# Optimization experiments

Hardware: AMD Instinct MI355X
Metric: run time of the kernel (lower is better)

Reference implementation:

```python
import jax, jax.numpy as jnp
import numpy as np

N_NODES = 20000
N_EDGES = 640000
D = 128          # vision_dim == topo_dim
OUT = 256        # out_dim
B = 64           # image batch == num graphs
HW = 64
NEG_SLOPE = 0.2


def _sn(w2d, u):
    """PyTorch spectral_norm forward: one power iteration (u,v detached), W/sigma."""
    v = jax.lax.stop_gradient(w2d.T @ u)
    v = v / (jnp.linalg.norm(v) + 1e-12)
    u2 = jax.lax.stop_gradient(w2d @ v)
    u2 = u2 / (jnp.linalg.norm(u2) + 1e-12)
    sigma = u2 @ (w2d @ v)
    return w2d / sigma


def _leaky(x):
    return jnp.where(x >= 0, x, NEG_SLOPE * x)


def setup_inputs() -> dict:
    key = jax.random.key(0)
    ks = jax.random.split(key, 16)
    vis = jax.random.normal(ks[0], (B, D, HW, HW), dtype=jnp.float32)
    topo = jax.random.normal(ks[1], (N_NODES, D), dtype=jnp.float32)
    edge_index = jax.random.randint(ks[2], (2, N_EDGES), 0, N_NODES, dtype=jnp.int64)
    batch = jnp.sort(jax.random.randint(ks[3], (N_NODES,), 0, B, dtype=jnp.int64))
    s = 0.05
    conv_w = jax.random.normal(ks[4], (D, D, 3, 3), dtype=jnp.float32) * s
    conv_b = jnp.zeros((D,), dtype=jnp.float32)
    conv_u = jax.random.normal(ks[5], (D,), dtype=jnp.float32)
    fcv_w = jax.random.normal(ks[6], (OUT, D * 4), dtype=jnp.float32) * s
    fcv_b = jnp.zeros((OUT,), dtype=jnp.float32)
    fcv_u = jax.random.normal(ks[7], (OUT,), dtype=jnp.float32)
    gcn_w = jax.random.normal(ks[8], (D, D), dtype=jnp.float32) * s
    gcn_b = jnp.zeros((D,), dtype=jnp.float32)
    fct_w = jax.random.normal(ks[9], (OUT, D), dtype=jnp.float32) * s
    fct_b = jnp.zeros((OUT,), dtype=jnp.float32)
    fct_u = jax.random.normal(ks[10], (OUT,), dtype=jnp.float32)
    return dict(vis=vis, topo=topo, edge_index=edge_index, batch=batch,
                conv_w=conv_w, conv_b=conv_b, conv_u=conv_u,
                fcv_w=fcv_w, fcv_b=fcv_b, fcv_u=fcv_u,
                gcn_w=gcn_w, gcn_b=gcn_b,
                fct_w=fct_w, fct_b=fct_b, fct_u=fct_u)


def reference(vis, topo, edge_index, batch,
              conv_w, conv_b, conv_u,
              fcv_w, fcv_b, fcv_u,
              gcn_w, gcn_b,
              fct_w, fct_b, fct_u):
    # ---- vision head: spectral-norm conv3x3 -> leaky_relu -> adaptive max pool 2x2 -> SN linear
    cw = _sn(conv_w.reshape(D, -1), conv_u).reshape(conv_w.shape)
    x = jax.lax.conv_general_dilated(vis, cw, window_strides=(1, 1), padding='VALID',
                                     dimension_numbers=('NCHW', 'OIHW', 'NCHW'))
    x = _leaky(x + conv_b[None, :, None, None])              # [B, D, 62, 62]
    Bc, C, H, W = x.shape
    x = x.reshape(Bc, C, 2, H // 2, 2, W // 2).max(axis=(3, 5))  # adaptive max pool -> [B,D,2,2]
    x = x.reshape(Bc, -1)                                    # [B, 4D]
    vis_score = x @ _sn(fcv_w, fcv_u).T + fcv_b              # [B, OUT]

    # ---- topo head: GCNConv (sym-norm, self-loops) -> leaky_relu -> global max pool -> SN linear
    n = topo.shape[0]
    loop = jnp.arange(n, dtype=edge_index.dtype)
    src = jnp.concatenate([edge_index[0], loop])
    dst = jnp.concatenate([edge_index[1], loop])
    deg = jax.ops.segment_sum(jnp.ones_like(dst, dtype=topo.dtype), dst, num_segments=n)
    dis = jnp.where(deg > 0, jax.lax.rsqrt(jnp.maximum(deg, 1.0)), 0.0)
    norm = dis[src] * dis[dst]                               # [E+N]
    xw = topo @ gcn_w                                        # [N, D]
    h = jax.ops.segment_sum(norm[:, None] * xw[src], dst, num_segments=n) + gcn_b
    h = _leaky(h)
    pooled = jax.ops.segment_max(h, batch, num_segments=B)   # [B, D]
    topo_score = pooled @ _sn(fct_w, fct_u).T + fct_b        # [B, OUT]

    return (vis_score, topo_score)
```

## Files before the change

kernel.cpp:

```cpp
#include <hip/hip_runtime.h>
#include <hip/hip_bf16.h>
#include <float.h>
#include <stdint.h>

#define NB   64
#define CD   128
#define OUTD 256
#define NNODE 20000
#define NEDGE 640000

typedef __bf16 bf16x8 __attribute__((ext_vector_type(8)));
typedef __bf16 bf16x4 __attribute__((ext_vector_type(4)));
typedef float  f32x4  __attribute__((ext_vector_type(4)));

__device__ inline void gl_lds16(const void* g, void* l) {
  __builtin_amdgcn_global_load_lds(
      (const __attribute__((address_space(1))) void*)g,
      (__attribute__((address_space(3))) void*)l, 16, 0, 0);
}

__device__ inline void atomicMaxF(float* addr, float val) {
  if (val >= 0.f) atomicMax((int*)addr, __float_as_int(val));
  else            atomicMin((unsigned int*)addr, __float_as_uint(val));
}

__global__ void k_init(float* __restrict__ pooled_v, float* __restrict__ pooled_t,
                       int* __restrict__ cnt, int* __restrict__ fill,
                       float* __restrict__ sn_scratch, int* __restrict__ ntotal) {
  const int i = blockIdx.x * 256 + threadIdx.x;
  if (i < NB * CD * 4) pooled_v[i] = -FLT_MAX;
  if (i < NB * CD)     pooled_t[i] = -FLT_MAX;
  if (i < NNODE)       { cnt[i] = 0; fill[i] = 0; }
  if (i < 1796)        sn_scratch[i] = 0.0f;
  if (i == 0)          *ntotal = 0;
}

__global__ __launch_bounds__(256) void k_sn_v(const float* __restrict__ conv_w, const float* __restrict__ conv_u,
                                              const float* __restrict__ fcv_w,  const float* __restrict__ fcv_u,
                                              const float* __restrict__ fct_w,  const float* __restrict__ fct_u,
                                              float* __restrict__ sn) {
  const int bb = blockIdx.x;
  const float* W; const float* u; float* v; int C; int r0;
  if (bb < 4)       { W = conv_w; u = conv_u; v = sn;        C = 1152; r0 = bb * 32; }
  else if (bb < 12) { W = fcv_w;  u = fcv_u;  v = sn + 1152; C = 512;  r0 = (bb - 4) * 32; }
  else              { W = fct_w;  u = fct_u;  v = sn + 1664; C = 128;  r0 = (bb - 12) * 32; }
  const int tid = threadIdx.x;
  float acc[5] = {0.f, 0.f, 0.f, 0.f, 0.f};
  for (int i = r0; i < r0 + 32; ++i) {
    const float ui = u[i];
    const float* row = W + (size_t)i * C;
    #pragma unroll
    for (int t = 0; t < 5; ++t) {
      const int j = tid + t * 256;
      if (j < C) acc[t] += ui * row[j];
    }
  }
  #pragma unroll
  for (int t = 0; t < 5; ++t) {
    const int j = tid + t * 256;
    if (j < C) atomicAdd(&v[j], acc[t]);
  }
}

__global__ __launch_bounds__(256) void k_sn_w(const float* __restrict__ conv_w,
                                              const float* __restrict__ fcv_w,
                                              const float* __restrict__ fct_w,
                                              float* __restrict__ sn) {
  const int gw = blockIdx.x * 4 + (threadIdx.x >> 6);
  const int lane = threadIdx.x & 63;
  const float* W; const float* v; int C, m, row;
  if (gw < 128)      { W = conv_w; v = sn;        C = 1152; m = 0; row = gw; }
  else if (gw < 384) { W = fcv_w;  v = sn + 1152; C = 512;  m = 1; row = gw - 128; }
  else               { W = fct_w;  v = sn + 1664; C = 128;  m = 2; row = gw - 384; }
  const float* wr = W + (size_t)row * C;
  float y = 0.f;
  for (int c = lane; c < C; c += 64) y += wr[c] * v[c];
  #pragma unroll
  for (int s = 32; s > 0; s >>= 1) y += __shfl_xor(y, s, 64);
  if (lane == 0) atomicAdd(&sn[1792 + m], y * y);
}

__global__ __launch_bounds__(256) void k_sn_fin(const float* __restrict__ sn, float* __restrict__ inv_sigma) {
  __shared__ float red[256];
  const int tid = threadIdx.x;
  const int off[4] = {0, 1152, 1664, 1792};
  for (int m = 0; m < 3; ++m) {
    const int C = off[m + 1] - off[m];
    float ss = 0.f;
    for (int j = tid; j < C; j += 256) { const float a = sn[off[m] + j]; ss += a * a; }
    red[tid] = ss; __syncthreads();
    for (int s = 128; s > 0; s >>= 1) { if (tid < s) red[tid] += red[tid + s]; __syncthreads(); }
    if (tid == 0) inv_sigma[m] = (sqrtf(red[0]) + 1e-12f) / sqrtf(sn[1792 + m]);
    __syncthreads();
  }
}

__global__ void k_pack(const float* __restrict__ conv_w, const float* __restrict__ inv_sigma,
                       __hip_bfloat16* __restrict__ Bt2) {
  const int t = blockIdx.x * 256 + threadIdx.x;
  if (t >= 147456) return;
  const int j = t & 7, n = (t >> 3) & 127, s = (t >> 10) & 7, hk = (t >> 13) & 1, tap = t >> 14;
  const int ci = hk * 64 + s * 8 + j;
  Bt2[t] = __float2bfloat16(conv_w[n * 1152 + ci * 9 + tap] * inv_sigma[0]);
}

__global__ __launch_bounds__(256) void k_transpose(const float* __restrict__ vis,
                                                   __hip_bfloat16* __restrict__ visT2) {
  __shared__ float tile[8192];
  const int by = blockIdx.x;
  const int b = by >> 6, y = by & 63;
  const int t = threadIdx.x;
  const float* src = vis + (size_t)b * 524288 + (size_t)(t >> 6) * 4096 + y * 64 + (t & 63);
  #pragma unroll
  for (int i = 0; i < 32; ++i)
    tile[(i * 4 + (t >> 6)) * 64 + (t & 63)] = src[(size_t)i * 4 * 4096];
  __syncthreads();
  bf16x8* dst = (bf16x8*)(visT2 + ((size_t)by << 13));
  #pragma unroll
  for (int k = 0; k < 4; ++k) {
    const int j = k * 256 + t;
    const int g = j >> 6, x = j & 63;
    union { bf16x8 v; __hip_bfloat16 h[8]; } u;
    #pragma unroll
    for (int cc = 0; cc < 8; ++cc)
      u.h[cc] = __float2bfloat16(tile[(g * 8 + cc) * 64 + x]);
    dst[j] = u.v;
  }
}

__global__ __launch_bounds__(256, 4) void k_conv(const __hip_bfloat16* __restrict__ visT2,
                                                 const __hip_bfloat16* __restrict__ Bt2,
                                                 const float* __restrict__ conv_b,
                                                 float* __restrict__ pooled_v) {
  __shared__ bf16x8 lds_a[1024];
  __shared__ bf16x8 lds_b[1024];
  const int bx = blockIdx.x;
  const int b = bx / 31;
  const int y0 = (bx - b * 31) * 2;
  const int tid = threadIdx.x;
  const int wave = tid >> 6, lane = tid & 63;
  const int quad = lane >> 4, l15 = lane & 15;

  f32x4 acc[8][2];
  #pragma unroll
  for (int i = 0; i < 8; ++i) {
    acc[i][0] = f32x4{0.f, 0.f, 0.f, 0.f};
    acc[i][1] = f32x4{0.f, 0.f, 0.f, 0.f};
  }

  const __hip_bfloat16* vb = visT2 + ((size_t)b << 19);
  const int s0 = wave << 1;
  bf16x8* ldsA0 = &lds_a[s0 << 7];
  bf16x8* ldsB0 = &lds_b[s0 << 7];
  const int lane8 = lane << 3;

  for (int ky = 0; ky < 3; ++ky) {
    for (int kx = 0; kx < 3; ++kx) {
      const int tap = ky * 3 + kx;
      #pragma unroll
      for (int hk = 0; hk < 2; ++hk) {
        const __hip_bfloat16* a0p = vb + ((size_t)(((y0 + ky) << 4) + (hk << 3) + s0) << 9) + (kx << 3) + lane8;
        const __hip_bfloat16* a1p = vb + ((size_t)(((y0 + 1 + ky) << 4) + (hk << 3) + s0) << 9) + (kx << 3) + lane8;
        const __hip_bfloat16* bp  = Bt2 + (((size_t)(((tap << 1) + hk) << 3) + s0) << 10) + lane8;
        gl_lds16(a0p,        ldsA0);
        gl_lds16(a1p,        ldsA0 + 64);
        gl_lds16(a0p + 512,  ldsA0 + 128);
        gl_lds16(a1p + 512,  ldsA0 + 192);
        gl_lds16(bp,         ldsB0);
        gl_lds16(bp + 512,   ldsB0 + 64);
        gl_lds16(bp + 1024,  ldsB0 + 128);
        gl_lds16(bp + 1536,  ldsB0 + 192);
        __syncthreads();
        const bf16x8 b00 = lds_b[(quad << 7) + (wave << 5) + l15];
        const bf16x8 b01 = lds_b[(quad << 7) + (wave << 5) + 16 + l15];
        const bf16x8 b10 = lds_b[((4 + quad) << 7) + (wave << 5) + l15];
        const bf16x8 b11 = lds_b[((4 + quad) << 7) + (wave << 5) + 16 + l15];
        #pragma unroll
        for (int mt = 0; mt < 8; ++mt) {
          const bf16x8 a0 = lds_a[(quad << 7) + (mt << 4) + l15];
          const bf16x8 a1 = lds_a[((4 + quad) << 7) + (mt << 4) + l15];
          acc[mt][0] = __builtin_amdgcn_mfma_f32_16x16x32_bf16(a0, b00, acc[mt][0], 0, 0, 0);
          acc[mt][1] = __builtin_amdgcn_mfma_f32_16x16x32_bf16(a0, b01, acc[mt][1], 0, 0, 0);
          acc[mt][0] = __builtin_amdgcn_mfma_f32_16x16x32_bf16(a1, b10, acc[mt][0], 0, 0, 0);
          acc[mt][1] = __builtin_amdgcn_mfma_f32_16x16x32_bf16(a1, b11, acc[mt][1], 0, 0, 0);
        }
        __syncthreads();
      }
    }
  }

  const float cb0 = conv_b[(wave << 5) + l15];
  const float cb1 = conv_b[(wave << 5) + 16 + l15];
  float pmax[2][2][2];
  #pragma unroll
  for (int i = 0; i < 8; ++i) (&pmax[0][0][0])[i] = -FLT_MAX;

  #pragma unroll
  for (int mt = 0; mt < 8; ++mt) {
    const int py = (y0 + (mt >> 2)) >= 31 ? 1 : 0;
    #pragma unroll
    for (int r = 0; r < 4; ++r) {
      const int x = ((mt & 3) << 4) + (quad << 2) + r;
      if (x < 62) {
        const int px = x >= 31 ? 1 : 0;
        float v0 = acc[mt][0][r] + cb0;  v0 = v0 >= 0.f ? v0 : 0.2f * v0;
        float v1 = acc[mt][1][r] + cb1;  v1 = v1 >= 0.f ? v1 : 0.2f * v1;
        pmax[0][py][px] = fmaxf(pmax[0][py][px], v0);
        pmax[1][py][px] = fmaxf(pmax[1][py][px], v1);
      }
    }
  }
  #pragma unroll
  for (int nt = 0; nt < 2; ++nt)
    #pragma unroll
    for (int py = 0; py < 2; ++py)
      #pragma unroll
      for (int px = 0; px < 2; ++px) {
        float v = pmax[nt][py][px];
        v = fmaxf(v, __shfl_xor(v, 16, 64));
        v = fmaxf(v, __shfl_xor(v, 32, 64));
        if (quad == 0) {
          const int n = (wave << 5) + (nt << 4) + l15;
          atomicMaxF(&pooled_v[(size_t)b * 512 + n * 4 + py * 2 + px], v);
        }
      }
}

__global__ void k_deg(const int* __restrict__ dst, int* __restrict__ cnt) {
  const int e = blockIdx.x * 256 + threadIdx.x;
  if (e < NEDGE) atomicAdd(&cnt[dst[e]], 1);
}

__global__ __launch_bounds__(256) void k_scan(const int* __restrict__ cnt, int* __restrict__ offset,
                                              int* __restrict__ total, float* __restrict__ dis) {
  __shared__ int red[256];
  __shared__ int sbase;
  const int tid = threadIdx.x;
  const int n = blockIdx.x * 256 + tid;
  const int v = (n < NNODE) ? cnt[n] : 0;
  red[tid] = v; __syncthreads();
  for (int d = 1; d < 256; d <<= 1) {
    const int t = (tid >= d) ? red[tid - d] : 0;
    __syncthreads();
    red[tid] += t;
    __syncthreads();
  }
  if (tid == 255) sbase = atomicAdd(total, red[255]);
  __syncthreads();
  if (n < NNODE) {
    offset[n] = sbase + red[tid] - v;
    dis[n] = rsqrtf((float)(v + 1));
  }
}

__global__ void k_bucket(const int* __restrict__ src, const int* __restrict__ dst,
                         const int* __restrict__ offset, int* __restrict__ fill,
                         int* __restrict__ sorted_src) {
  const int e = blockIdx.x * 256 + threadIdx.x;
  if (e >= NEDGE) return;
  const int t = dst[e];
  const int pos = atomicAdd(&fill[t], 1);
  sorted_src[offset[t] + pos] = src[e];
}

__global__ __launch_bounds__(256) void k_xw(const float* __restrict__ topo, const float* __restrict__ gcn_w,
                                            const float* __restrict__ dis, __bf16* __restrict__ xws) {
  __shared__ f32x4 w4[4096];
  const int tid = threadIdx.x;
  const f32x4* gw4 = (const f32x4*)gcn_w;
  for (int i = tid; i < 4096; i += 256) w4[i] = gw4[i];
  __syncthreads();
  const int n0 = blockIdx.x * 64;
  const int jq = tid & 31, ns = tid >> 5;
  for (int pass = 0; pass < 8; ++pass) {
    const int n = n0 + pass * 8 + ns;
    if (n >= NNODE) break;
    const f32x4* tr4 = (const f32x4*)(topo + (size_t)n * 128);
    f32x4 a = {0.f, 0.f, 0.f, 0.f};
    for (int d4 = 0; d4 < 32; ++d4) {
      const f32x4 t = tr4[d4];
      const int base = (d4 << 7) + jq;
      #pragma unroll
      for (int m = 0; m < 4; ++m) {
        const f32x4 w = w4[base + m * 32];
        #pragma unroll
        for (int k = 0; k < 4; ++k) a[k] += t[m] * w[k];
      }
    }
    const float dn = dis[n];
    bf16x4 o;
    #pragma unroll
    for (int k = 0; k < 4; ++k) o[k] = (__bf16)(a[k] * dn);
    ((bf16x4*)xws)[(size_t)n * 32 + jq] = o;
  }
}

__global__ __launch_bounds__(256) void k_gather(const int* __restrict__ sorted_src,
                                                const int* __restrict__ offset, const int* __restrict__ cnt,
                                                const float* __restrict__ dis, const __bf16* __restrict__ xws,
                                                const float* __restrict__ gcn_b, __bf16* __restrict__ h) {
  const int wave = threadIdx.x >> 6, lane = threadIdx.x & 63;
  const int n = blockIdx.x * 4 + wave;
  const int slot = lane >> 4, l16 = lane & 15;
  const int e0 = offset[n], ne = cnt[n];
  const bf16x8* x8 = (const bf16x8*)xws;
  float a[8];
  if (slot == 0) {
    const bf16x8 v = x8[(size_t)n * 16 + l16];
    #pragma unroll
    for (int k = 0; k < 8; ++k) a[k] = (float)v[k];
  } else {
    #pragma unroll
    for (int k = 0; k < 8; ++k) a[k] = 0.f;
  }
  for (int e = slot; e < ne; e += 4) {
    const int s = sorted_src[e0 + e];
    const bf16x8 v = x8[(size_t)s * 16 + l16];
    #pragma unroll
    for (int k = 0; k < 8; ++k) a[k] += (float)v[k];
  }
  #pragma unroll
  for (int k = 0; k < 8; ++k) {
    a[k] += __shfl_xor(a[k], 16, 64);
    a[k] += __shfl_xor(a[k], 32, 64);
  }
  if (slot == 0) {
    const float dn = dis[n];
    bf16x8 o;
    #pragma unroll
    for (int k = 0; k < 8; ++k) {
      float t = gcn_b[(l16 << 3) + k] + dn * a[k];
      t = t >= 0.f ? t : 0.2f * t;
      o[k] = (__bf16)t;
    }
    ((bf16x8*)h)[(size_t)n * 16 + l16] = o;
  }
}

__global__ void k_pool_t(const __bf16* __restrict__ h, const int* __restrict__ batch,
                         float* __restrict__ pooled_t) {
  const int d = threadIdx.x;
  const int n0 = blockIdx.x * 32;
  float run = -FLT_MAX;
  int cur = batch[n0];
  for (int i = 0; i < 32; ++i) {
    const int n = n0 + i;
    const int g = batch[n];
    if (g != cur) {
      atomicMaxF(&pooled_t[cur * 128 + d], run);
      run = -FLT_MAX; cur = g;
    }
    run = fmaxf(run, (float)h[(size_t)n * 128 + d]);
  }
  atomicMaxF(&pooled_t[cur * 128 + d], run);
}

__global__ __launch_bounds__(256) void k_fc(const float* __restrict__ pooled_v, const float* __restrict__ fcv_w,
                                            const float* __restrict__ fcv_b,
                                            const float* __restrict__ pooled_t, const float* __restrict__ fct_w,
                                            const float* __restrict__ fct_b,
                                            const float* __restrict__ inv_sigma, float* __restrict__ out) {
  const int tid = threadIdx.x;
  if (blockIdx.x < 64) {
    __shared__ f32x4 xr[128];
    const int b = blockIdx.x;
    if (tid < 128) xr[tid] = ((const f32x4*)pooled_v)[b * 128 + tid];
    __syncthreads();
    const f32x4* wr = (const f32x4*)(fcv_w + (size_t)tid * 512);
    f32x4 a4 = {0.f, 0.f, 0.f, 0.f};
    for (int f = 0; f < 128; ++f) {
      const f32x4 x = xr[f];
      const f32x4 w = wr[f];
      #pragma unroll
      for (int k = 0; k < 4; ++k) a4[k] += x[k] * w[k];
    }
    const float a = a4[0] + a4[1] + a4[2] + a4[3];
    out[b * 256 + tid] = a * inv_sigma[1] + fcv_b[tid];
  } else {
    __shared__ f32x4 xr2[32];
    const int b = blockIdx.x - 64;
    if (tid < 32) xr2[tid] = ((const f32x4*)pooled_t)[b * 32 + tid];
    __syncthreads();
    const f32x4* wr = (const f32x4*)(fct_w + (size_t)tid * 128);
    f32x4 a4 = {0.f, 0.f, 0.f, 0.f};
    for (int f = 0; f < 32; ++f) {
      const f32x4 x = xr2[f];
      const f32x4 w = wr[f];
      #pragma unroll
      for (int k = 0; k < 4; ++k) a4[k] += x[k] * w[k];
    }
    const float a = a4[0] + a4[1] + a4[2] + a4[3];
    out[NB * 256 + b * 256 + tid] = a * inv_sigma[2] + fct_b[tid];
  }
}

extern "C" void kernel_launch(void* const* d_in, const int* in_sizes, int n_in,
                              void* d_out, int out_size, void* d_ws, size_t ws_size,
                              hipStream_t stream) {
  const float* vis    = (const float*)d_in[0];
  const float* topo   = (const float*)d_in[1];
  const int*   eidx   = (const int*)d_in[2];
  const int*   batch  = (const int*)d_in[3];
  const float* conv_w = (const float*)d_in[4];
  const float* conv_b = (const float*)d_in[5];
  const float* conv_u = (const float*)d_in[6];
  const float* fcv_w  = (const float*)d_in[7];
  const float* fcv_b  = (const float*)d_in[8];
  const float* fcv_u  = (const float*)d_in[9];
  const float* gcn_w  = (const float*)d_in[10];
  const float* gcn_b  = (const float*)d_in[11];
  const float* fct_w  = (const float*)d_in[12];
  const float* fct_b  = (const float*)d_in[13];
  const float* fct_u  = (const float*)d_in[14];
  float* out = (float*)d_out;

  char* p = (char*)d_ws;
  float* inv_sigma  = (float*)p; p += 256;
  float* sn_scratch = (float*)p; p += 1796 * 4 + 240;
  float* pooled_v   = (float*)p; p += (size_t)NB * 512 * 4;
  float* pooled_t   = (float*)p; p += (size_t)NB * 128 * 4;
  int*   cnt        = (int*)p;   p += (size_t)NNODE * 4;
  int*   offset     = (int*)p;   p += (size_t)NNODE * 4;
  int*   fill       = (int*)p;   p += (size_t)NNODE * 4;
  float* dis        = (float*)p; p += (size_t)NNODE * 4;
  int*   ntotal     = (int*)p;   p += 256;
  int*   sorted_src = (int*)p;   p += (size_t)NEDGE * 4;
  __bf16* xws       = (__bf16*)p; p += (size_t)NNODE * 128 * 2 + 256;
  __bf16* h         = (__bf16*)p; p += (size_t)NNODE * 128 * 2 + 256;
  __hip_bfloat16* Bt2 = (__hip_bfloat16*)p; p += (size_t)147456 * 2;
  p = (char*)(((uintptr_t)p + 255) & ~(uintptr_t)255);
  __hip_bfloat16* visT2 = (__hip_bfloat16*)p;

  hipLaunchKernelGGL(k_init,      dim3(128),   dim3(256), 0, stream, pooled_v, pooled_t, cnt, fill, sn_scratch, ntotal);
  hipLaunchKernelGGL(k_sn_v,      dim3(20),    dim3(256), 0, stream, conv_w, conv_u, fcv_w, fcv_u, fct_w, fct_u, sn_scratch);
  hipLaunchKernelGGL(k_sn_w,      dim3(160),   dim3(256), 0, stream, conv_w, fcv_w, fct_w, sn_scratch);
  hipLaunchKernelGGL(k_sn_fin,    dim3(1),     dim3(256), 0, stream, sn_scratch, inv_sigma);
  hipLaunchKernelGGL(k_pack,      dim3(576),   dim3(256), 0, stream, conv_w, inv_sigma, Bt2);
  hipLaunchKernelGGL(k_transpose, dim3(4096),  dim3(256), 0, stream, vis, visT2);
  hipLaunchKernelGGL(k_conv,      dim3(64*31), dim3(256), 0, stream, visT2, Bt2, conv_b, pooled_v);
  hipLaunchKernelGGL(k_deg,       dim3(2500),  dim3(256), 0, stream, eidx + NEDGE, cnt);
  hipLaunchKernelGGL(k_scan,      dim3(79),    dim3(256), 0, stream, cnt, offset, ntotal, dis);
  hipLaunchKernelGGL(k_bucket,    dim3(2500),  dim3(256), 0, stream, eidx, eidx + NEDGE, offset, fill, sorted_src);
  hipLaunchKernelGGL(k_xw,        dim3(313),   dim3(256), 0, stream, topo, gcn_w, dis, xws);
  hipLaunchKernelGGL(k_gather,    dim3(5000),  dim3(256), 0, stream, sorted_src, offset, cnt, dis, xws, gcn_b, h);
  hipLaunchKernelGGL(k_pool_t,    dim3(625),   dim3(128), 0, stream, h, batch, pooled_t);
  hipLaunchKernelGGL(k_fc,        dim3(128),   dim3(256), 0, stream, pooled_v, fcv_w, fcv_b, pooled_t, fct_w, fct_b, inv_sigma, out);
}
```

Before: 554.6 us.

## Merge prep, pack, degree and scan/xw kernels; vectorize transpose loads; swizzle conv blocks

```diff
diff --git a/kernel.cpp b/kernel.cpp
--- a/kernel.cpp
+++ b/kernel.cpp
@@ -95,36 +95,44 @@
   }
 }
 
-__global__ void k_pack(const float* __restrict__ conv_w, const float* __restrict__ inv_sigma,
-                       __hip_bfloat16* __restrict__ Bt2) {
-  const int t = blockIdx.x * 256 + threadIdx.x;
-  if (t >= 147456) return;
-  const int j = t & 7, n = (t >> 3) & 127, s = (t >> 10) & 7, hk = (t >> 13) & 1, tap = t >> 14;
-  const int ci = hk * 64 + s * 8 + j;
-  Bt2[t] = __float2bfloat16(conv_w[n * 1152 + ci * 9 + tap] * inv_sigma[0]);
-}
-
-__global__ __launch_bounds__(256) void k_transpose(const float* __restrict__ vis,
-                                                   __hip_bfloat16* __restrict__ visT2) {
+__global__ __launch_bounds__(256) void k_prep(const float* __restrict__ vis, __hip_bfloat16* __restrict__ visT2,
+                                              const float* __restrict__ conv_w, const float* __restrict__ inv_sigma,
+                                              __hip_bfloat16* __restrict__ Bt2,
+                                              const int* __restrict__ dst, int* __restrict__ cnt) {
   __shared__ float tile[8192];
-  const int by = blockIdx.x;
-  const int b = by >> 6, y = by & 63;
+  const int bid = blockIdx.x;
   const int t = threadIdx.x;
-  const float* src = vis + (size_t)b * 524288 + (size_t)(t >> 6) * 4096 + y * 64 + (t & 63);
-  #pragma unroll
-  for (int i = 0; i < 32; ++i)
-    tile[(i * 4 + (t >> 6)) * 64 + (t & 63)] = src[(size_t)i * 4 * 4096];
-  __syncthreads();
-  bf16x8* dst = (bf16x8*)(visT2 + ((size_t)by << 13));
-  #pragma unroll
-  for (int k = 0; k < 4; ++k) {
-    const int j = k * 256 + t;
-    const int g = j >> 6, x = j & 63;
-    union { bf16x8 v; __hip_bfloat16 h[8]; } u;
-    #pragma unroll
-    for (int cc = 0; cc < 8; ++cc)
-      u.h[cc] = __float2bfloat16(tile[(g * 8 + cc) * 64 + x]);
-    dst[j] = u.v;
+  if (bid < 4096) {
+    const int b = bid >> 6, y = bid & 63;
+    const int c0 = t >> 4, x4 = (t & 15) << 2;
+    const float* src = vis + (size_t)b * 524288 + y * 64;
+    #pragma unroll
+    for (int i = 0; i < 8; ++i) {
+      const int c = i * 16 + c0;
+      *(f32x4*)&tile[c * 64 + x4] = *(const f32x4*)(src + (size_t)c * 4096 + x4);
+    }
+    __syncthreads();
+    bf16x8* dstv = (bf16x8*)(visT2 + ((size_t)bid << 13));
+    #pragma unroll
+    for (int k = 0; k < 4; ++k) {
+      const int j = k * 256 + t;
+      const int g = j >> 6, x = j & 63;
+      union { bf16x8 v; __hip_bfloat16 h[8]; } u;
+      #pragma unroll
+      for (int cc = 0; cc < 8; ++cc)
+        u.h[cc] = __float2bfloat16(tile[(g * 8 + cc) * 64 + x]);
+      dstv[j] = u.v;
+    }
+  } else if (bid < 4672) {
+    const int tt = (bid - 4096) * 256 + t;
+    if (tt < 147456) {
+      const int j = tt & 7, n = (tt >> 3) & 127, s = (tt >> 10) & 7, hk = (tt >> 13) & 1, tap = tt >> 14;
+      const int ci = hk * 64 + s * 8 + j;
+      Bt2[tt] = __float2bfloat16(conv_w[n * 1152 + ci * 9 + tap] * inv_sigma[0]);
+    }
+  } else {
+    const int e = (bid - 4672) * 256 + t;
+    if (e < NEDGE) atomicAdd(&cnt[dst[e]], 1);
   }
 }
 
@@ -134,7 +142,7 @@
                                                  float* __restrict__ pooled_v) {
   __shared__ bf16x8 lds_a[1024];
   __shared__ bf16x8 lds_b[1024];
-  const int bx = blockIdx.x;
+  const int bx = (blockIdx.x & 7) * 248 + (blockIdx.x >> 3);
   const int b = bx / 31;
   const int y0 = (bx - b * 31) * 2;
   const int tid = threadIdx.x;
@@ -226,30 +234,57 @@
       }
 }
 
-__global__ void k_deg(const int* __restrict__ dst, int* __restrict__ cnt) {
-  const int e = blockIdx.x * 256 + threadIdx.x;
-  if (e < NEDGE) atomicAdd(&cnt[dst[e]], 1);
-}
-
-__global__ __launch_bounds__(256) void k_scan(const int* __restrict__ cnt, int* __restrict__ offset,
-                                              int* __restrict__ total, float* __restrict__ dis) {
-  __shared__ int red[256];
+__global__ __launch_bounds__(256) void k_scan_xw(const int* __restrict__ cnt, int* __restrict__ offset,
+                                                 int* __restrict__ total, float* __restrict__ dis,
+                                                 const float* __restrict__ topo, const float* __restrict__ gcn_w,
+                                                 __bf16* __restrict__ xws) {
+  __shared__ f32x4 w4[4096];
   __shared__ int sbase;
   const int tid = threadIdx.x;
-  const int n = blockIdx.x * 256 + tid;
-  const int v = (n < NNODE) ? cnt[n] : 0;
-  red[tid] = v; __syncthreads();
-  for (int d = 1; d < 256; d <<= 1) {
-    const int t = (tid >= d) ? red[tid - d] : 0;
-    __syncthreads();
-    red[tid] += t;
-    __syncthreads();
-  }
-  if (tid == 255) sbase = atomicAdd(total, red[255]);
-  __syncthreads();
-  if (n < NNODE) {
-    offset[n] = sbase + red[tid] - v;
-    dis[n] = rsqrtf((float)(v + 1));
+  if (blockIdx.x < 79) {
+    int* red = (int*)w4;
+    const int n = blockIdx.x * 256 + tid;
+    const int v = (n < NNODE) ? cnt[n] : 0;
+    red[tid] = v; __syncthreads();
+    for (int d = 1; d < 256; d <<= 1) {
+      const int t = (tid >= d) ? red[tid - d] : 0;
+      __syncthreads();
+      red[tid] += t;
+      __syncthreads();
+    }
+    if (tid == 255) sbase = atomicAdd(total, red[255]);
+    __syncthreads();
+    if (n < NNODE) {
+      offset[n] = sbase + red[tid] - v;
+      dis[n] = rsqrtf((float)(v + 1));
+    }
+  } else {
+    const f32x4* gw4 = (const f32x4*)gcn_w;
+    for (int i = tid; i < 4096; i += 256) w4[i] = gw4[i];
+    __syncthreads();
+    const int n0 = (blockIdx.x - 79) * 64;
+    const int jq = tid & 31, ns = tid >> 5;
+    for (int pass = 0; pass < 8; ++pass) {
+      const int n = n0 + pass * 8 + ns;
+      if (n >= NNODE) break;
+      const f32x4* tr4 = (const f32x4*)(topo + (size_t)n * 128);
+      f32x4 a = {0.f, 0.f, 0.f, 0.f};
+      for (int d4 = 0; d4 < 32; ++d4) {
+        const f32x4 t = tr4[d4];
+        const int base = (d4 << 7) + jq;
+        #pragma unroll
+        for (int m = 0; m < 4; ++m) {
+          const f32x4 w = w4[base + m * 32];
+          #pragma unroll
+          for (int k = 0; k < 4; ++k) a[k] += t[m] * w[k];
+        }
+      }
+      const float dn = rsqrtf((float)(cnt[n] + 1));
+      bf16x4 o;
+      #pragma unroll
+      for (int k = 0; k < 4; ++k) o[k] = (__bf16)(a[k] * dn);
+      ((bf16x4*)xws)[(size_t)n * 32 + jq] = o;
+    }
   }
 }
 
@@ -261,38 +296,6 @@
   const int t = dst[e];
   const int pos = atomicAdd(&fill[t], 1);
   sorted_src[offset[t] + pos] = src[e];
-}
-
-__global__ __launch_bounds__(256) void k_xw(const float* __restrict__ topo, const float* __restrict__ gcn_w,
-                                            const float* __restrict__ dis, __bf16* __restrict__ xws) {
-  __shared__ f32x4 w4[4096];
-  const int tid = threadIdx.x;
-  const f32x4* gw4 = (const f32x4*)gcn_w;
-  for (int i = tid; i < 4096; i += 256) w4[i] = gw4[i];
-  __syncthreads();
-  const int n0 = blockIdx.x * 64;
-  const int jq = tid & 31, ns = tid >> 5;
-  for (int pass = 0; pass < 8; ++pass) {
-    const int n = n0 + pass * 8 + ns;
-    if (n >= NNODE) break;
-    const f32x4* tr4 = (const f32x4*)(topo + (size_t)n * 128);
-    f32x4 a = {0.f, 0.f, 0.f, 0.f};
-    for (int d4 = 0; d4 < 32; ++d4) {
-      const f32x4 t = tr4[d4];
-      const int base = (d4 << 7) + jq;
-      #pragma unroll
-      for (int m = 0; m < 4; ++m) {
-        const f32x4 w = w4[base + m * 32];
-        #pragma unroll
-        for (int k = 0; k < 4; ++k) a[k] += t[m] * w[k];
-      }
-    }
-    const float dn = dis[n];
-    bf16x4 o;
-    #pragma unroll
-    for (int k = 0; k < 4; ++k) o[k] = (__bf16)(a[k] * dn);
-    ((bf16x4*)xws)[(size_t)n * 32 + jq] = o;
-  }
 }
 
 __global__ __launch_bounds__(256) void k_gather(const int* __restrict__ sorted_src,
@@ -431,18 +434,15 @@
   p = (char*)(((uintptr_t)p + 255) & ~(uintptr_t)255);
   __hip_bfloat16* visT2 = (__hip_bfloat16*)p;
 
-  hipLaunchKernelGGL(k_init,      dim3(128),   dim3(256), 0, stream, pooled_v, pooled_t, cnt, fill, sn_scratch, ntotal);
-  hipLaunchKernelGGL(k_sn_v,      dim3(20),    dim3(256), 0, stream, conv_w, conv_u, fcv_w, fcv_u, fct_w, fct_u, sn_scratch);
-  hipLaunchKernelGGL(k_sn_w,      dim3(160),   dim3(256), 0, stream, conv_w, fcv_w, fct_w, sn_scratch);
-  hipLaunchKernelGGL(k_sn_fin,    dim3(1),     dim3(256), 0, stream, sn_scratch, inv_sigma);
-  hipLaunchKernelGGL(k_pack,      dim3(576),   dim3(256), 0, stream, conv_w, inv_sigma, Bt2);
-  hipLaunchKernelGGL(k_transpose, dim3(4096),  dim3(256), 0, stream, vis, visT2);
-  hipLaunchKernelGGL(k_conv,      dim3(64*31), dim3(256), 0, stream, visT2, Bt2, conv_b, pooled_v);
-  hipLaunchKernelGGL(k_deg,       dim3(2500),  dim3(256), 0, stream, eidx + NEDGE, cnt);
-  hipLaunchKernelGGL(k_scan,      dim3(79),    dim3(256), 0, stream, cnt, offset, ntotal, dis);
-  hipLaunchKernelGGL(k_bucket,    dim3(2500),  dim3(256), 0, stream, eidx, eidx + NEDGE, offset, fill, sorted_src);
-  hipLaunchKernelGGL(k_xw,        dim3(313),   dim3(256), 0, stream, topo, gcn_w, dis, xws);
-  hipLaunchKernelGGL(k_gather,    dim3(5000),  dim3(256), 0, stream, sorted_src, offset, cnt, dis, xws, gcn_b, h);
-  hipLaunchKernelGGL(k_pool_t,    dim3(625),   dim3(128), 0, stream, h, batch, pooled_t);
-  hipLaunchKernelGGL(k_fc,        dim3(128),   dim3(256), 0, stream, pooled_v, fcv_w, fcv_b, pooled_t, fct_w, fct_b, inv_sigma, out);
-}
+  hipLaunchKernelGGL(k_init,    dim3(128),  dim3(256), 0, stream, pooled_v, pooled_t, cnt, fill, sn_scratch, ntotal);
+  hipLaunchKernelGGL(k_sn_v,    dim3(20),   dim3(256), 0, stream, conv_w, conv_u, fcv_w, fcv_u, fct_w, fct_u, sn_scratch);
+  hipLaunchKernelGGL(k_sn_w,    dim3(160),  dim3(256), 0, stream, conv_w, fcv_w, fct_w, sn_scratch);
+  hipLaunchKernelGGL(k_sn_fin,  dim3(1),    dim3(256), 0, stream, sn_scratch, inv_sigma);
+  hipLaunchKernelGGL(k_prep,    dim3(7172), dim3(256), 0, stream, vis, visT2, conv_w, inv_sigma, Bt2, eidx + NEDGE, cnt);
+  hipLaunchKernelGGL(k_conv,    dim3(64*31), dim3(256), 0, stream, visT2, Bt2, conv_b, pooled_v);
+  hipLaunchKernelGGL(k_scan_xw, dim3(392),  dim3(256), 0, stream, cnt, offset, ntotal, dis, topo, gcn_w, xws);
+  hipLaunchKernelGGL(k_bucket,  dim3(2500), dim3(256), 0, stream, eidx, eidx + NEDGE, offset, fill, sorted_src);
+  hipLaunchKernelGGL(k_gather,  dim3(5000), dim3(256), 0, stream, sorted_src, offset, cnt, dis, xws, gcn_b, h);
+  hipLaunchKernelGGL(k_pool_t,  dim3(625),  dim3(128), 0, stream, h, batch, pooled_t);
+  hipLaunchKernelGGL(k_fc,      dim3(128),  dim3(256), 0, stream, pooled_v, fcv_w, fcv_b, pooled_t, fct_w, fct_b, inv_sigma, out);
+}
```

Result: no change. 546.3 us (-1.5%).
